# Kernel tuning notes

Hardware: AMD Instinct MI355X
Metric: run time of the kernel (lower is better)

## Reference

```python
import jax, jax.numpy as jnp
import numpy as np

N_NODES = 50000
N_EDGES = 500000
N_RELS = 460
D = 128
N_LAYERS = 2
RRELU_SLOPE = (1.0 / 8.0 + 1.0 / 3.0) / 2.0  # F.rrelu eval-mode negative slope


def setup_inputs() -> dict:
    key = jax.random.key(0)
    ks = jax.random.split(key, 9)
    return {
        "node_feats": jax.random.normal(ks[0], (N_NODES, D), dtype=jnp.float32),
        "rel_emb": jax.random.normal(ks[1], (N_RELS, D), dtype=jnp.float32),
        "norm": jax.random.uniform(ks[2], (N_NODES, 1), dtype=jnp.float32),
        "edge_src": jax.random.randint(ks[3], (N_EDGES,), 0, N_NODES, dtype=jnp.int32),
        "edge_dst": jax.random.randint(ks[4], (N_EDGES,), 0, N_NODES, dtype=jnp.int32),
        "edge_rel": jax.random.randint(ks[5], (N_EDGES,), 0, N_RELS, dtype=jnp.int32),
        "W_neigh": jax.random.normal(ks[6], (N_LAYERS, D, D), dtype=jnp.float32) * 0.05,
        "W_loop": jax.random.normal(ks[7], (N_LAYERS, D, D), dtype=jnp.float32) * 0.05,
        "W_evolve": jax.random.normal(ks[8], (N_LAYERS, D, D), dtype=jnp.float32) * 0.05,
    }


def reference(node_feats, rel_emb, norm, edge_src, edge_dst, edge_rel,
              W_neigh, W_loop, W_evolve):
    """RGCNCell with 2 UnionRGCNLayers (eval mode, dropout off)."""
    n = node_feats.shape[0]
    # nodes with in-degree > 0 use loop_weight, others evolve_loop_weight
    indeg = jax.ops.segment_sum(jnp.ones_like(edge_dst, dtype=node_feats.dtype),
                                edge_dst, num_segments=n)
    has_in = (indeg > 0)[:, None]  # [N,1]

    h = node_feats
    for l in range(W_neigh.shape[0]):
        # self-loop message: choose weight per node by in-degree mask
        loop_msg = jnp.where(has_in, h @ W_loop[l], h @ W_evolve[l])  # [N,D]
        # message: gather src h + relation emb, transform  (gather-GEMM)
        msg = (h[edge_src] + rel_emb[edge_rel]) @ W_neigh[l]  # [E,D]
        # scatter-sum to dst, then apply per-node norm (apply_func)
        agg = jax.ops.segment_sum(msg, edge_dst, num_segments=n) * norm  # [N,D]
        h = agg + loop_msg
        # F.rrelu in eval mode == leaky relu with slope (lower+upper)/2
        h = jnp.where(h >= 0, h, RRELU_SLOPE * h)
    return h
```

## Files before the change

kernel.cpp:

```cpp
#include <hip/hip_runtime.h>

#define DD 128
#define CAP 64
static constexpr float SLOPE = (1.0f/8.0f + 1.0f/3.0f) * 0.5f;

typedef __attribute__((ext_vector_type(8))) short bf16x8;
typedef __attribute__((ext_vector_type(4))) float f32x4;

__device__ inline unsigned short f2bf(float x) {
    unsigned u = __builtin_bit_cast(unsigned, x);
    unsigned r = (u + 0x7FFFu + ((u >> 16) & 1u)) >> 16;
    return (unsigned short)r;
}
__device__ inline float bflo(unsigned u) {
    unsigned v = u << 16; return __builtin_bit_cast(float, v);
}
__device__ inline float bfhi(unsigned u) {
    unsigned v = u & 0xFFFF0000u; return __builtin_bit_cast(float, v);
}
__device__ inline float2 bf2f2(unsigned u) {
    return make_float2(bflo(u), bfhi(u));
}

__global__ __launch_bounds__(256) void init_k(
    const float* __restrict__ Wn, const float* __restrict__ Wl,
    const float* __restrict__ node, const float* __restrict__ rel_emb,
    unsigned short* __restrict__ Wt, int* __restrict__ slots,
    unsigned short* __restrict__ hbf, int N, int R, int NB)
{
    int b = blockIdx.x;
    if (b < 64) {
        int i = b * 256 + threadIdx.x;
        int l = i >> 13;
        int rem = i & 8191;
        int n = rem >> 5;
        int k0 = (rem & 31) * 4;
        const float* src = (n < 128) ? (Wn + l * DD * DD + n)
                                     : (Wl + l * DD * DD + (n - 128));
        unsigned short o0 = f2bf(src[(k0 + 0) * DD]);
        unsigned short o1 = f2bf(src[(k0 + 1) * DD]);
        unsigned short o2 = f2bf(src[(k0 + 2) * DD]);
        unsigned short o3 = f2bf(src[(k0 + 3) * DD]);
        *(ushort4*)&Wt[((size_t)l * 256 + n) * DD + k0] = make_ushort4(o0, o1, o2, o3);
    } else if (b < 64 + NB) {
        int i = (b - 64) * 256 + threadIdx.x;
        if (i < N) slots[i] = 0;
    } else {
        long c = (long)(b - 64 - NB) * 256 + threadIdx.x;
        long total = (long)(N + R) * 16;
        if (c >= total) return;
        long r = c >> 4;
        int  ch = (int)(c & 15);
        const float* s = (r < N) ? (node + r * DD + ch * 8)
                                 : (rel_emb + (r - N) * DD + ch * 8);
        float4 v0 = *(const float4*)s;
        float4 v1 = *(const float4*)(s + 4);
        union { bf16x8 v; unsigned short u[8]; } t;
        t.u[0] = f2bf(v0.x); t.u[1] = f2bf(v0.y);
        t.u[2] = f2bf(v0.z); t.u[3] = f2bf(v0.w);
        t.u[4] = f2bf(v1.x); t.u[5] = f2bf(v1.y);
        t.u[6] = f2bf(v1.z); t.u[7] = f2bf(v1.w);
        *(bf16x8*)&hbf[r * DD + ch * 8] = t.v;
    }
}

__global__ __launch_bounds__(256) void fill_k(const int* __restrict__ esrc,
                                              const int* __restrict__ edst,
                                              const int* __restrict__ erel,
                                              int* __restrict__ slots,
                                              int* __restrict__ spack, int E) {
    int e = blockIdx.x * 256 + threadIdx.x;
    if (e >= E) return;
    int d = edst[e];
    int slot = atomicAdd(&slots[d], 1);
    if (slot < CAP) spack[(size_t)d * CAP + slot] = esrc[e] | (erel[e] << 17);
}

__global__ __launch_bounds__(256) void gemm_dual_mfma_k(
    const unsigned short* __restrict__ Abf,
    const unsigned short* __restrict__ Wt,
    unsigned short* __restrict__ hWn,
    unsigned short* __restrict__ loopm,
    unsigned short* __restrict__ rW,
    int N, int M)
{
    __shared__ unsigned short Wsm[256 * DD];
    int tid = threadIdx.x;
    int row0 = blockIdx.x * 64;
    int w = tid >> 6, lane = tid & 63;
    int g = lane >> 4, q = lane & 15;

    bf16x8 a[4][4];
    #pragma unroll
    for (int s = 0; s < 4; ++s)
        #pragma unroll
        for (int mi = 0; mi < 4; ++mi) {
            int r = row0 + mi * 16 + q;
            if (r >= M) r = M - 1;
            a[s][mi] = *(const bf16x8*)&Abf[(size_t)r * DD + s * 32 + g * 8];
        }

    #pragma unroll
    for (int it = 0; it < 16; ++it) {
        int ci = it * 256 + tid;
        uint4 wv = *(const uint4*)((const char*)Wt + (size_t)ci * 16);
        int lin = ci * 16;
        int row = lin >> 8;
        int off = lin ^ ((row & 7) << 4);
        *(uint4*)((char*)Wsm + off) = wv;
    }
    __syncthreads();

    int sw = (q & 7) << 4;
    f32x4 acc[4][4];
    #pragma unroll
    for (int mi = 0; mi < 4; ++mi)
        #pragma unroll
        for (int ni = 0; ni < 4; ++ni)
            acc[mi][ni] = (f32x4){0.f, 0.f, 0.f, 0.f};

    #pragma unroll
    for (int s = 0; s < 4; ++s) {
        int off = 64 * s + 16 * g;
        bf16x8 b[4];
        #pragma unroll
        for (int ni = 0; ni < 4; ++ni) {
            int n = w * 64 + ni * 16 + q;
            b[ni] = *(const bf16x8*)((const char*)Wsm + n * 256 + (off ^ sw));
        }
        #pragma unroll
        for (int mi = 0; mi < 4; ++mi)
            #pragma unroll
            for (int ni = 0; ni < 4; ++ni)
                acc[mi][ni] = __builtin_amdgcn_mfma_f32_16x16x32_bf16(
                    a[s][mi], b[ni], acc[mi][ni], 0, 0, 0);
    }
    __syncthreads();

    char* Cb = (char*)Wsm;
    #pragma unroll
    for (int mi = 0; mi < 4; ++mi)
        #pragma unroll
        for (int ni = 0; ni < 4; ++ni) {
            int col = w * 64 + ni * 16 + q;
            #pragma unroll
            for (int j = 0; j < 4; ++j) {
                int row = mi * 16 + g * 4 + j;
                int off = row * 512 + ((col * 2) ^ (((row >> 2) & 7) << 5));
                *(unsigned short*)(Cb + off) = f2bf(acc[mi][ni][j]);
            }
        }
    __syncthreads();

    #pragma unroll
    for (int c0 = 0; c0 < 8; ++c0) {
        int c = c0 * 256 + tid;
        int row = c >> 5, colc = c & 31;
        int off = row * 512 + ((colc * 16) ^ (((row >> 2) & 7) << 5));
        bf16x8 v = *(const bf16x8*)(Cb + off);
        int grow = row0 + row;
        int col = colc * 8;
        if (grow < N) {
            if (col < DD) *(bf16x8*)&hWn[(size_t)grow * DD + col] = v;
            else          *(bf16x8*)&loopm[(size_t)grow * DD + col - DD] = v;
        } else if (grow < M && col < DD) {
            *(bf16x8*)&rW[(size_t)(grow - N) * DD + col] = v;
        }
    }
}

#define ACC8(A, B) do { \
    acc0 += bf2f2((A).x) + bf2f2((B).x); \
    acc1 += bf2f2((A).y) + bf2f2((B).y); \
    acc2 += bf2f2((A).z) + bf2f2((B).z); \
    acc3 += bf2f2((A).w) + bf2f2((B).w); \
} while (0)

template<bool LAYER1>
__global__ __launch_bounds__(256) void aggregate_k(
    const unsigned short* __restrict__ hWn, const unsigned short* __restrict__ rW,
    const int* __restrict__ spack,
    const int* __restrict__ counts,
    const unsigned short* __restrict__ loopm, const float* __restrict__ norm,
    const unsigned short* __restrict__ hbf,
    const float* __restrict__ We,
    unsigned short* __restrict__ hbf_out,
    float* __restrict__ fout,
    int N)
{
    int t = blockIdx.x * 256 + threadIdx.x;
    int r = t >> 5;
    if (r >= N) return;
    int eg = (t >> 4) & 1;
    int sl = t & 15;
    int cnt = counts[r];
    size_t boff = (size_t)sl * 16;

    float2 acc0 = make_float2(0.f, 0.f), acc1 = acc0, acc2 = acc0, acc3 = acc0;

    if (cnt == 0) {
        for (int k = eg * 64; k < eg * 64 + 64; ++k) {
            float hk = bflo((unsigned)hbf[(size_t)r * DD + k]);
            const float* wr = We + (size_t)k * DD + sl * 8;
            float4 w0 = *(const float4*)wr;
            float4 w1 = *(const float4*)(wr + 4);
            acc0.x += hk * w0.x; acc0.y += hk * w0.y;
            acc1.x += hk * w0.z; acc1.y += hk * w0.w;
            acc2.x += hk * w1.x; acc2.y += hk * w1.y;
            acc3.x += hk * w1.z; acc3.y += hk * w1.w;
        }
    } else {
        const char* hb = (const char*)hWn;
        const char* rb = (const char*)rW;
        int beg = r * CAP;
        int end = beg + cnt;
        int i = beg + eg;
        for (; i + 2 < end; i += 4) {
            int p0 = spack[i], p1 = spack[i + 2];
            uint4 a0 = *(const uint4*)(hb + (size_t)(p0 & 0x1FFFF) * 256 + boff);
            uint4 b0 = *(const uint4*)(rb + (size_t)(p0 >> 17) * 256 + boff);
            uint4 a1 = *(const uint4*)(hb + (size_t)(p1 & 0x1FFFF) * 256 + boff);
            uint4 b1 = *(const uint4*)(rb + (size_t)(p1 >> 17) * 256 + boff);
            ACC8(a0, b0); ACC8(a1, b1);
        }
        if (i < end) {
            int p0 = spack[i];
            uint4 a0 = *(const uint4*)(hb + (size_t)(p0 & 0x1FFFF) * 256 + boff);
            uint4 b0 = *(const uint4*)(rb + (size_t)(p0 >> 17) * 256 + boff);
            ACC8(a0, b0);
        }
    }

    acc0.x += __shfl_xor(acc0.x, 16); acc0.y += __shfl_xor(acc0.y, 16);
    acc1.x += __shfl_xor(acc1.x, 16); acc1.y += __shfl_xor(acc1.y, 16);
    acc2.x += __shfl_xor(acc2.x, 16); acc2.y += __shfl_xor(acc2.y, 16);
    acc3.x += __shfl_xor(acc3.x, 16); acc3.y += __shfl_xor(acc3.y, 16);

    float o[8];
    if (cnt == 0) {
        o[0] = acc0.x; o[1] = acc0.y; o[2] = acc1.x; o[3] = acc1.y;
        o[4] = acc2.x; o[5] = acc2.y; o[6] = acc3.x; o[7] = acc3.y;
    } else {
        float nv = norm[r];
        uint4 lu = *(const uint4*)((const char*)loopm + (size_t)r * 256 + boff);
        o[0] = acc0.x * nv + bflo(lu.x);
        o[1] = acc0.y * nv + bfhi(lu.x);
        o[2] = acc1.x * nv + bflo(lu.y);
        o[3] = acc1.y * nv + bfhi(lu.y);
        o[4] = acc2.x * nv + bflo(lu.z);
        o[5] = acc2.y * nv + bfhi(lu.z);
        o[6] = acc3.x * nv + bflo(lu.w);
        o[7] = acc3.y * nv + bfhi(lu.w);
    }

    #pragma unroll
    for (int j = 0; j < 8; ++j) o[j] = o[j] >= 0.f ? o[j] : SLOPE * o[j];

    if (eg != 0) return;

    if constexpr (LAYER1) {
        union { bf16x8 v; unsigned short u[8]; } t2;
        #pragma unroll
        for (int j = 0; j < 8; ++j) t2.u[j] = f2bf(o[j]);
        *(bf16x8*)&hbf_out[(size_t)r * DD + sl * 8] = t2.v;
    } else {
        float* op = &fout[(size_t)r * DD + sl * 8];
        *(float4*)op       = make_float4(o[0], o[1], o[2], o[3]);
        *(float4*)(op + 4) = make_float4(o[4], o[5], o[6], o[7]);
    }
}

extern "C" void kernel_launch(void* const* d_in, const int* in_sizes, int n_in,
                              void* d_out, int out_size, void* d_ws, size_t ws_size,
                              hipStream_t stream) {
    const float* node    = (const float*)d_in[0];
    const float* rel_emb = (const float*)d_in[1];
    const float* norm    = (const float*)d_in[2];
    const int*   esrc    = (const int*)d_in[3];
    const int*   edst    = (const int*)d_in[4];
    const int*   erel    = (const int*)d_in[5];
    const float* Wn      = (const float*)d_in[6];
    const float* Wl      = (const float*)d_in[7];
    const float* We      = (const float*)d_in[8];
    int N = in_sizes[0] / DD;
    int R = in_sizes[1] / DD;
    int E = in_sizes[3];
    float* out = (float*)d_out;

    char* w = (char*)d_ws;
    auto alloc = [&](size_t bytes) {
        void* p = (void*)w;
        w += (bytes + 255) & ~(size_t)255;
        return p;
    };
    int*            slots  = (int*)           alloc((size_t)N * 4);
    int*            spack  = (int*)           alloc((size_t)N * CAP * 4);
    unsigned short* Wt     = (unsigned short*)alloc((size_t)2 * 256 * DD * 2);
    unsigned short* rW     = (unsigned short*)alloc((size_t)R * DD * 2);
    unsigned short* hWn    = (unsigned short*)alloc((size_t)N * DD * 2);
    unsigned short* loopm  = (unsigned short*)alloc((size_t)N * DD * 2);
    unsigned short* hbf    = (unsigned short*)alloc((size_t)(N + R) * DD * 2);

    int NB = (N + 255) / 256;
    int CB = (int)(((long)(N + R) * 16 + 255) / 256);
    int M = N + R;

    init_k<<<64 + NB + CB, 256, 0, stream>>>(Wn, Wl, node, rel_emb,
                                             Wt, slots, hbf, N, R, NB);
    fill_k<<<(E + 255) / 256, 256, 0, stream>>>(esrc, edst, erel, slots, spack, E);

    int gemm_blocks = (M + 63) / 64;
    int agg_blocks  = (N * 32 + 255) / 256;

    gemm_dual_mfma_k<<<gemm_blocks, 256, 0, stream>>>(
        hbf, Wt, hWn, loopm, rW, N, M);
    aggregate_k<true><<<agg_blocks, 256, 0, stream>>>(
        hWn, rW, spack, slots, loopm, norm, hbf, We, hbf, nullptr, N);

    gemm_dual_mfma_k<<<gemm_blocks, 256, 0, stream>>>(
        hbf, Wt + (size_t)256 * DD, hWn, loopm, rW, N, M);
    aggregate_k<false><<<agg_blocks, 256, 0, stream>>>(
        hWn, rW, spack, slots, loopm, norm, hbf,
        We + (size_t)DD * DD, nullptr, out, N);
}
```

Measured before the change: 124.6 us.

## Fuse fp32-to-bf16 input conversion into GEMM and widen aggregation to 4 edge groups

Removes the separate bf16 conversion pass over node features and relation embeddings in the init kernel; the GEMM now loads fp32 inputs and converts them on the fly, and relation rows are always converted from fp32. The aggregation kernel now uses 64 threads per node (4 edge groups instead of 2), reduced with an extra cross-lane shuffle, to expose more memory-level parallelism for the gather. Layer-1 evolve rows read fp32 node features directly. The cost is more shuffles and more threads per low-degree node, plus the work of redundant conversion inside the GEMM.

```diff
diff --git a/kernel.cpp b/kernel.cpp
--- a/kernel.cpp
+++ b/kernel.cpp
@@ -21,12 +21,20 @@
 __device__ inline float2 bf2f2(unsigned u) {
     return make_float2(bflo(u), bfhi(u));
 }
+__device__ inline bf16x8 cvt8(const float* s) {
+    float4 v0 = *(const float4*)s;
+    float4 v1 = *(const float4*)(s + 4);
+    union { bf16x8 v; unsigned short u[8]; } t;
+    t.u[0] = f2bf(v0.x); t.u[1] = f2bf(v0.y);
+    t.u[2] = f2bf(v0.z); t.u[3] = f2bf(v0.w);
+    t.u[4] = f2bf(v1.x); t.u[5] = f2bf(v1.y);
+    t.u[6] = f2bf(v1.z); t.u[7] = f2bf(v1.w);
+    return t.v;
+}
 
 __global__ __launch_bounds__(256) void init_k(
     const float* __restrict__ Wn, const float* __restrict__ Wl,
-    const float* __restrict__ node, const float* __restrict__ rel_emb,
-    unsigned short* __restrict__ Wt, int* __restrict__ slots,
-    unsigned short* __restrict__ hbf, int N, int R, int NB)
+    unsigned short* __restrict__ Wt, int* __restrict__ slots, int N)
 {
     int b = blockIdx.x;
     if (b < 64) {
@@ -42,25 +50,9 @@
         unsigned short o2 = f2bf(src[(k0 + 2) * DD]);
         unsigned short o3 = f2bf(src[(k0 + 3) * DD]);
         *(ushort4*)&Wt[((size_t)l * 256 + n) * DD + k0] = make_ushort4(o0, o1, o2, o3);
-    } else if (b < 64 + NB) {
+    } else {
         int i = (b - 64) * 256 + threadIdx.x;
         if (i < N) slots[i] = 0;
-    } else {
-        long c = (long)(b - 64 - NB) * 256 + threadIdx.x;
-        long total = (long)(N + R) * 16;
-        if (c >= total) return;
-        long r = c >> 4;
-        int  ch = (int)(c & 15);
-        const float* s = (r < N) ? (node + r * DD + ch * 8)
-                                 : (rel_emb + (r - N) * DD + ch * 8);
-        float4 v0 = *(const float4*)s;
-        float4 v1 = *(const float4*)(s + 4);
-        union { bf16x8 v; unsigned short u[8]; } t;
-        t.u[0] = f2bf(v0.x); t.u[1] = f2bf(v0.y);
-        t.u[2] = f2bf(v0.z); t.u[3] = f2bf(v0.w);
-        t.u[4] = f2bf(v1.x); t.u[5] = f2bf(v1.y);
-        t.u[6] = f2bf(v1.z); t.u[7] = f2bf(v1.w);
-        *(bf16x8*)&hbf[r * DD + ch * 8] = t.v;
     }
 }
 
@@ -76,8 +68,10 @@
     if (slot < CAP) spack[(size_t)d * CAP + slot] = esrc[e] | (erel[e] << 17);
 }
 
+template<bool BF16IN>
 __global__ __launch_bounds__(256) void gemm_dual_mfma_k(
-    const unsigned short* __restrict__ Abf,
+    const void* __restrict__ hsrc,
+    const float* __restrict__ rel,
     const unsigned short* __restrict__ Wt,
     unsigned short* __restrict__ hWn,
     unsigned short* __restrict__ loopm,
@@ -97,7 +91,15 @@
         for (int mi = 0; mi < 4; ++mi) {
             int r = row0 + mi * 16 + q;
             if (r >= M) r = M - 1;
-            a[s][mi] = *(const bf16x8*)&Abf[(size_t)r * DD + s * 32 + g * 8];
+            if (r < N) {
+                if constexpr (BF16IN)
+                    a[s][mi] = *(const bf16x8*)((const unsigned short*)hsrc
+                                + (size_t)r * DD + s * 32 + g * 8);
+                else
+                    a[s][mi] = cvt8((const float*)hsrc + (size_t)r * DD + s * 32 + g * 8);
+            } else {
+                a[s][mi] = cvt8(rel + (size_t)(r - N) * DD + s * 32 + g * 8);
+            }
         }
 
     #pragma unroll
@@ -182,6 +184,7 @@
     const int* __restrict__ spack,
     const int* __restrict__ counts,
     const unsigned short* __restrict__ loopm, const float* __restrict__ norm,
+    const float* __restrict__ node,
     const unsigned short* __restrict__ hbf,
     const float* __restrict__ We,
     unsigned short* __restrict__ hbf_out,
@@ -189,9 +192,9 @@
     int N)
 {
     int t = blockIdx.x * 256 + threadIdx.x;
-    int r = t >> 5;
+    int r = t >> 6;
     if (r >= N) return;
-    int eg = (t >> 4) & 1;
+    int eg = (t >> 4) & 3;
     int sl = t & 15;
     int cnt = counts[r];
     size_t boff = (size_t)sl * 16;
@@ -199,8 +202,10 @@
     float2 acc0 = make_float2(0.f, 0.f), acc1 = acc0, acc2 = acc0, acc3 = acc0;
 
     if (cnt == 0) {
-        for (int k = eg * 64; k < eg * 64 + 64; ++k) {
-            float hk = bflo((unsigned)hbf[(size_t)r * DD + k]);
+        for (int k = eg * 32; k < eg * 32 + 32; ++k) {
+            float hk;
+            if constexpr (LAYER1) hk = node[(size_t)r * DD + k];
+            else                  hk = bflo((unsigned)hbf[(size_t)r * DD + k]);
             const float* wr = We + (size_t)k * DD + sl * 8;
             float4 w0 = *(const float4*)wr;
             float4 w1 = *(const float4*)(wr + 4);
@@ -215,8 +220,8 @@
         int beg = r * CAP;
         int end = beg + cnt;
         int i = beg + eg;
-        for (; i + 2 < end; i += 4) {
-            int p0 = spack[i], p1 = spack[i + 2];
+        for (; i + 4 < end; i += 8) {
+            int p0 = spack[i], p1 = spack[i + 4];
             uint4 a0 = *(const uint4*)(hb + (size_t)(p0 & 0x1FFFF) * 256 + boff);
             uint4 b0 = *(const uint4*)(rb + (size_t)(p0 >> 17) * 256 + boff);
             uint4 a1 = *(const uint4*)(hb + (size_t)(p1 & 0x1FFFF) * 256 + boff);
@@ -235,6 +240,12 @@
     acc1.x += __shfl_xor(acc1.x, 16); acc1.y += __shfl_xor(acc1.y, 16);
     acc2.x += __shfl_xor(acc2.x, 16); acc2.y += __shfl_xor(acc2.y, 16);
     acc3.x += __shfl_xor(acc3.x, 16); acc3.y += __shfl_xor(acc3.y, 16);
+    acc0.x += __shfl_xor(acc0.x, 32); acc0.y += __shfl_xor(acc0.y, 32);
+    acc1.x += __shfl_xor(acc1.x, 32); acc1.y += __shfl_xor(acc1.y, 32);
+    acc2.x += __shfl_xor(acc2.x, 32); acc2.y += __shfl_xor(acc2.y, 32);
+    acc3.x += __shfl_xor(acc3.x, 32); acc3.y += __shfl_xor(acc3.y, 32);
+
+    if (eg != 0) return;
 
     float o[8];
     if (cnt == 0) {
@@ -255,8 +266,6 @@
 
     #pragma unroll
     for (int j = 0; j < 8; ++j) o[j] = o[j] >= 0.f ? o[j] : SLOPE * o[j];
-
-    if (eg != 0) return;
 
     if constexpr (LAYER1) {
         union { bf16x8 v; unsigned short u[8]; } t2;
@@ -299,27 +308,25 @@
     unsigned short* rW     = (unsigned short*)alloc((size_t)R * DD * 2);
     unsigned short* hWn    = (unsigned short*)alloc((size_t)N * DD * 2);
     unsigned short* loopm  = (unsigned short*)alloc((size_t)N * DD * 2);
-    unsigned short* hbf    = (unsigned short*)alloc((size_t)(N + R) * DD * 2);
+    unsigned short* hbf    = (unsigned short*)alloc((size_t)N * DD * 2);
 
     int NB = (N + 255) / 256;
-    int CB = (int)(((long)(N + R) * 16 + 255) / 256);
     int M = N + R;
 
-    init_k<<<64 + NB + CB, 256, 0, stream>>>(Wn, Wl, node, rel_emb,
-                                             Wt, slots, hbf, N, R, NB);
+    init_k<<<64 + NB, 256, 0, stream>>>(Wn, Wl, Wt, slots, N);
     fill_k<<<(E + 255) / 256, 256, 0, stream>>>(esrc, edst, erel, slots, spack, E);
 
     int gemm_blocks = (M + 63) / 64;
-    int agg_blocks  = (N * 32 + 255) / 256;
-
-    gemm_dual_mfma_k<<<gemm_blocks, 256, 0, stream>>>(
-        hbf, Wt, hWn, loopm, rW, N, M);
+    int agg_blocks  = (N * 64 + 255) / 256;
+
+    gemm_dual_mfma_k<false><<<gemm_blocks, 256, 0, stream>>>(
+        node, rel_emb, Wt, hWn, loopm, rW, N, M);
     aggregate_k<true><<<agg_blocks, 256, 0, stream>>>(
-        hWn, rW, spack, slots, loopm, norm, hbf, We, hbf, nullptr, N);
-
-    gemm_dual_mfma_k<<<gemm_blocks, 256, 0, stream>>>(
-        hbf, Wt + (size_t)256 * DD, hWn, loopm, rW, N, M);
+        hWn, rW, spack, slots, loopm, norm, node, nullptr, We, hbf, nullptr, N);
+
+    gemm_dual_mfma_k<true><<<gemm_blocks, 256, 0, stream>>>(
+        hbf, rel_emb, Wt + (size_t)256 * DD, hWn, loopm, rW, N, M);
     aggregate_k<false><<<agg_blocks, 256, 0, stream>>>(
-        hWn, rW, spack, slots, loopm, norm, hbf,
+        hWn, rW, spack, slots, loopm, norm, nullptr, hbf,
         We + (size_t)DD * DD, nullptr, out, N);
 }
```

New measurement: 144.8 us. +16.2%, slower.
